# Kernel optimization log

Measured on AMD Instinct MI355X. Metric: run time of the kernel, lower is better.

## Reference

```python
import jax, jax.numpy as jnp
import numpy as np

RANK = 4
IN_FEATURES = 1024
OUT_FEATURES = 1024
ALPHA = 1.0
SCALING = ALPHA / RANK


def setup_inputs() -> dict:
    key = jax.random.key(0)
    kx, ka = jax.random.split(key)
    x = jax.random.normal(kx, (4, 8192, IN_FEATURES), dtype=jnp.float32)
    # kaiming_uniform_(a=sqrt(5)) on [rank, in_features]: bound = sqrt(3) * gain / sqrt(fan_in)
    # gain = sqrt(2/(1+a^2)) = sqrt(1/3); fan_in = in_features -> bound = 1/sqrt(in_features)
    bound = 1.0 / np.sqrt(IN_FEATURES)
    lora_A = jax.random.uniform(ka, (RANK, IN_FEATURES), dtype=jnp.float32, minval=-bound, maxval=bound)
    # original init is zeros for B; use random values so the output/gradients are non-trivial
    lora_B = jax.random.normal(jax.random.fold_in(key, 7), (OUT_FEATURES, RANK), dtype=jnp.float32) * 0.02
    return {"x": x, "lora_A": lora_A, "lora_B": lora_B}


def reference(x, lora_A, lora_B):
    # h = scaling * (x @ A^T) @ B^T   (dropout p=0 -> identity)
    h = jnp.einsum('bsi,ri->bsr', x, lora_A)      # [B, S, rank]
    h = jnp.einsum('bsr,or->bso', h, lora_B)      # [B, S, out_features]
    return h * SCALING
```

## Files before the change

### kernel.cpp

```cpp
#include <hip/hip_runtime.h>

#define IN_F 1024
#define OUT_F 1024
#define RANK 4
#define SCALING 0.25f
#define WAVES_PER_BLOCK 4
#define ROWS_PER_WAVE 8

__global__ __launch_bounds__(256, 2) void lora_fused(
    const float* __restrict__ x, const float* __restrict__ A,
    const float* __restrict__ B, float* __restrict__ out, int nrows) {
  const int lane = threadIdx.x & 63;
  const int wave = threadIdx.x >> 6;
  const int wave_id = blockIdx.x * WAVES_PER_BLOCK + wave;
  const int row0 = wave_id * ROWS_PER_WAVE;
  if (row0 >= nrows) return;

  const float4* __restrict__ A4 = (const float4*)A;
  float4 af[RANK][4];
#pragma unroll
  for (int r = 0; r < RANK; ++r)
#pragma unroll
    for (int w = 0; w < 4; ++w)
      af[r][w] = A4[r * 256 + w * 64 + lane];

  const float4* __restrict__ B4 = (const float4*)B;
  float4 bf[4][4];
#pragma unroll
  for (int w = 0; w < 4; ++w)
#pragma unroll
    for (int j = 0; j < 4; ++j)
      bf[w][j] = B4[4 * (w * 64 + lane) + j];

  float4 xv[4];
  {
    const float4* __restrict__ x4 = (const float4*)(x + (size_t)row0 * IN_F);
#pragma unroll
    for (int w = 0; w < 4; ++w) xv[w] = x4[w * 64 + lane];
  }

#pragma unroll 1
  for (int i = 0; i < ROWS_PER_WAVE; ++i) {
    const int row = row0 + i;
    if (row >= nrows) break;

    float4 xn[4];
    const bool have_next = (i + 1 < ROWS_PER_WAVE) && (row + 1 < nrows);
    if (have_next) {
      const float4* __restrict__ x4n =
          (const float4*)(x + (size_t)(row + 1) * IN_F);
#pragma unroll
      for (int w = 0; w < 4; ++w) xn[w] = x4n[w * 64 + lane];
    }

    float h[RANK];
#pragma unroll
    for (int r = 0; r < RANK; ++r) h[r] = 0.0f;
#pragma unroll
    for (int r = 0; r < RANK; ++r)
#pragma unroll
      for (int w = 0; w < 4; ++w)
        h[r] += xv[w].x * af[r][w].x + xv[w].y * af[r][w].y +
                xv[w].z * af[r][w].z + xv[w].w * af[r][w].w;

#pragma unroll
    for (int off = 32; off > 0; off >>= 1)
#pragma unroll
      for (int r = 0; r < RANK; ++r) h[r] += __shfl_xor(h[r], off, 64);

#pragma unroll
    for (int r = 0; r < RANK; ++r) h[r] *= SCALING;

    float4* __restrict__ out4 = (float4*)(out + (size_t)row * OUT_F);
#pragma unroll
    for (int w = 0; w < 4; ++w) {
      float4 res;
      res.x = h[0] * bf[w][0].x + h[1] * bf[w][0].y + h[2] * bf[w][0].z +
              h[3] * bf[w][0].w;
      res.y = h[0] * bf[w][1].x + h[1] * bf[w][1].y + h[2] * bf[w][1].z +
              h[3] * bf[w][1].w;
      res.z = h[0] * bf[w][2].x + h[1] * bf[w][2].y + h[2] * bf[w][2].z +
              h[3] * bf[w][2].w;
      res.w = h[0] * bf[w][3].x + h[1] * bf[w][3].y + h[2] * bf[w][3].z +
              h[3] * bf[w][3].w;
      out4[w * 64 + lane] = res;
    }

    if (have_next) {
#pragma unroll
      for (int w = 0; w < 4; ++w) xv[w] = xn[w];
    }
  }
}

extern "C" void kernel_launch(void* const* d_in, const int* in_sizes, int n_in,
                              void* d_out, int out_size, void* d_ws,
                              size_t ws_size, hipStream_t stream) {
  const float* x = (const float*)d_in[0];
  const float* A = (const float*)d_in[1];
  const float* B = (const float*)d_in[2];
  float* out = (float*)d_out;

  const int nrows = in_sizes[0] / IN_F;
  const int waves = (nrows + ROWS_PER_WAVE - 1) / ROWS_PER_WAVE;
  const int blocks = (waves + WAVES_PER_BLOCK - 1) / WAVES_PER_BLOCK;
  lora_fused<<<blocks, WAVES_PER_BLOCK * 64, 0, stream>>>(x, A, B, out, nrows);
}
```

Baseline: 235.3 us.

## Stage x tiles into LDS via async global_load_lds with double buffering

Restructures the kernel so each block handles a 16-row tile. x rows are streamed into LDS in 256-column chunks using the global_load_lds builtin, with double buffering and explicit waitcnt. A is kept in LDS, and the rank-4 projection is reduced over 16-lane groups. The up-projection then writes the full tile using B held in registers. The intent is to raise memory-level parallelism on the x read and to spread output writes across the whole block. The risks are hand-coded waitcnt encodings, ROW_PITCH padding alignment for the 16-byte LDS loads, and no tail handling when nrows is not a multiple of 16.

```diff
diff --git a/kernel.cpp b/kernel.cpp
--- a/kernel.cpp
+++ b/kernel.cpp
@@ -1,95 +1,116 @@
 #include <hip/hip_runtime.h>
+#include <stdint.h>
 
 #define IN_F 1024
 #define OUT_F 1024
-#define RANK 4
 #define SCALING 0.25f
-#define WAVES_PER_BLOCK 4
-#define ROWS_PER_WAVE 8
+#define TILE_ROWS 16
+#define CHUNK_COLS 256
+#define NCHUNK (IN_F / CHUNK_COLS)
+#define ROW_PITCH 260
+#define BLOCK 256
 
-__global__ __launch_bounds__(256, 2) void lora_fused(
+typedef __attribute__((address_space(3))) unsigned int as3_u32;
+typedef const __attribute__((address_space(1))) unsigned int as1_u32;
+
+__device__ __forceinline__ void row_to_lds(const float* g, const float* lds_row,
+                                           int lane) {
+  __builtin_amdgcn_global_load_lds(
+      (as1_u32*)(uintptr_t)(g + lane * 4),
+      (as3_u32*)(uint32_t)(uintptr_t)(lds_row),
+      16, 0, 0);
+}
+
+__global__ __launch_bounds__(BLOCK) void lora_tile(
     const float* __restrict__ x, const float* __restrict__ A,
     const float* __restrict__ B, float* __restrict__ out, int nrows) {
-  const int lane = threadIdx.x & 63;
-  const int wave = threadIdx.x >> 6;
-  const int wave_id = blockIdx.x * WAVES_PER_BLOCK + wave;
-  const int row0 = wave_id * ROWS_PER_WAVE;
+  __shared__ float4 As4[4 * 256];
+  __shared__ float xs[2][TILE_ROWS * ROW_PITCH];
+  __shared__ float4 hf[TILE_ROWS];
+
+  const int t = threadIdx.x;
+  const int lane = t & 63;
+  const int wave = t >> 6;
+  const int row0 = blockIdx.x * TILE_ROWS;
   if (row0 >= nrows) return;
 
+  const float4* __restrict__ B4 = (const float4*)B;
+  const float4 bf0 = B4[4 * t + 0];
+  const float4 bf1 = B4[4 * t + 1];
+  const float4 bf2 = B4[4 * t + 2];
+  const float4 bf3 = B4[4 * t + 3];
+
   const float4* __restrict__ A4 = (const float4*)A;
-  float4 af[RANK][4];
 #pragma unroll
-  for (int r = 0; r < RANK; ++r)
+  for (int k = 0; k < 4; ++k) As4[t + 256 * k] = A4[t + 256 * k];
+  __syncthreads();
+
 #pragma unroll
-    for (int w = 0; w < 4; ++w)
-      af[r][w] = A4[r * 256 + w * 64 + lane];
-
-  const float4* __restrict__ B4 = (const float4*)B;
-  float4 bf[4][4];
-#pragma unroll
-  for (int w = 0; w < 4; ++w)
-#pragma unroll
-    for (int j = 0; j < 4; ++j)
-      bf[w][j] = B4[4 * (w * 64 + lane) + j];
-
-  float4 xv[4];
-  {
-    const float4* __restrict__ x4 = (const float4*)(x + (size_t)row0 * IN_F);
-#pragma unroll
-    for (int w = 0; w < 4; ++w) xv[w] = x4[w * 64 + lane];
+  for (int r = 0; r < 4; ++r) {
+    const int row = wave * 4 + r;
+    row_to_lds(x + (size_t)(row0 + row) * IN_F, &xs[0][row * ROW_PITCH], lane);
   }
 
-#pragma unroll 1
-  for (int i = 0; i < ROWS_PER_WAVE; ++i) {
-    const int row = row0 + i;
-    if (row >= nrows) break;
+  const int lrow = lane >> 4;
+  const int seg = lane & 15;
+  const int myrow = wave * 4 + lrow;
 
-    float4 xn[4];
-    const bool have_next = (i + 1 < ROWS_PER_WAVE) && (row + 1 < nrows);
-    if (have_next) {
-      const float4* __restrict__ x4n =
-          (const float4*)(x + (size_t)(row + 1) * IN_F);
-#pragma unroll
-      for (int w = 0; w < 4; ++w) xn[w] = x4n[w * 64 + lane];
-    }
-
-    float h[RANK];
-#pragma unroll
-    for (int r = 0; r < RANK; ++r) h[r] = 0.0f;
-#pragma unroll
-    for (int r = 0; r < RANK; ++r)
-#pragma unroll
-      for (int w = 0; w < 4; ++w)
-        h[r] += xv[w].x * af[r][w].x + xv[w].y * af[r][w].y +
-                xv[w].z * af[r][w].z + xv[w].w * af[r][w].w;
+  float h0 = 0.f, h1 = 0.f, h2 = 0.f, h3 = 0.f;
 
 #pragma unroll
-    for (int off = 32; off > 0; off >>= 1)
+  for (int c = 0; c < NCHUNK; ++c) {
+    if (c + 1 < NCHUNK) {
 #pragma unroll
-      for (int r = 0; r < RANK; ++r) h[r] += __shfl_xor(h[r], off, 64);
+      for (int r = 0; r < 4; ++r) {
+        const int row = wave * 4 + r;
+        row_to_lds(x + (size_t)(row0 + row) * IN_F + (c + 1) * CHUNK_COLS,
+                   &xs[(c + 1) & 1][row * ROW_PITCH], lane);
+      }
+      __builtin_amdgcn_s_waitcnt(0xF74);
+    } else {
+      __builtin_amdgcn_s_waitcnt(0xF70);
+    }
+    __asm__ __volatile__("" ::: "memory");
+
+    const float4* __restrict__ xr4 =
+        (const float4*)&xs[c & 1][myrow * ROW_PITCH + seg * 16];
+#pragma unroll
+    for (int j = 0; j < 4; ++j) {
+      const float4 xv = xr4[j];
+      const int ai = c * 64 + seg * 4 + j;
+      const float4 a0 = As4[0 * 256 + ai];
+      const float4 a1 = As4[1 * 256 + ai];
+      const float4 a2 = As4[2 * 256 + ai];
+      const float4 a3 = As4[3 * 256 + ai];
+      h0 += xv.x * a0.x + xv.y * a0.y + xv.z * a0.z + xv.w * a0.w;
+      h1 += xv.x * a1.x + xv.y * a1.y + xv.z * a1.z + xv.w * a1.w;
+      h2 += xv.x * a2.x + xv.y * a2.y + xv.z * a2.z + xv.w * a2.w;
+      h3 += xv.x * a3.x + xv.y * a3.y + xv.z * a3.z + xv.w * a3.w;
+    }
+  }
 
 #pragma unroll
-    for (int r = 0; r < RANK; ++r) h[r] *= SCALING;
+  for (int off = 1; off < 16; off <<= 1) {
+    h0 += __shfl_xor(h0, off, 64);
+    h1 += __shfl_xor(h1, off, 64);
+    h2 += __shfl_xor(h2, off, 64);
+    h3 += __shfl_xor(h3, off, 64);
+  }
+  if (seg == 0)
+    hf[myrow] = make_float4(h0 * SCALING, h1 * SCALING, h2 * SCALING,
+                            h3 * SCALING);
+  __syncthreads();
 
-    float4* __restrict__ out4 = (float4*)(out + (size_t)row * OUT_F);
+  float4* __restrict__ out4 = (float4*)out;
 #pragma unroll
-    for (int w = 0; w < 4; ++w) {
-      float4 res;
-      res.x = h[0] * bf[w][0].x + h[1] * bf[w][0].y + h[2] * bf[w][0].z +
-              h[3] * bf[w][0].w;
-      res.y = h[0] * bf[w][1].x + h[1] * bf[w][1].y + h[2] * bf[w][1].z +
-              h[3] * bf[w][1].w;
-      res.z = h[0] * bf[w][2].x + h[1] * bf[w][2].y + h[2] * bf[w][2].z +
-              h[3] * bf[w][2].w;
-      res.w = h[0] * bf[w][3].x + h[1] * bf[w][3].y + h[2] * bf[w][3].z +
-              h[3] * bf[w][3].w;
-      out4[w * 64 + lane] = res;
-    }
-
-    if (have_next) {
-#pragma unroll
-      for (int w = 0; w < 4; ++w) xv[w] = xn[w];
-    }
+  for (int r = 0; r < TILE_ROWS; ++r) {
+    const float4 h = hf[r];
+    float4 res;
+    res.x = h.x * bf0.x + h.y * bf0.y + h.z * bf0.z + h.w * bf0.w;
+    res.y = h.x * bf1.x + h.y * bf1.y + h.z * bf1.z + h.w * bf1.w;
+    res.z = h.x * bf2.x + h.y * bf2.y + h.z * bf2.z + h.w * bf2.w;
+    res.w = h.x * bf3.x + h.y * bf3.y + h.z * bf3.z + h.w * bf3.w;
+    out4[(size_t)(row0 + r) * (OUT_F / 4) + t] = res;
   }
 }
 
@@ -102,7 +123,6 @@
   float* out = (float*)d_out;
 
   const int nrows = in_sizes[0] / IN_F;
-  const int waves = (nrows + ROWS_PER_WAVE - 1) / ROWS_PER_WAVE;
-  const int blocks = (waves + WAVES_PER_BLOCK - 1) / WAVES_PER_BLOCK;
-  lora_fused<<<blocks, WAVES_PER_BLOCK * 64, 0, stream>>>(x, A, B, out, nrows);
+  const int blocks = (nrows + TILE_ROWS - 1) / TILE_ROWS;
+  lora_tile<<<blocks, BLOCK, 0, stream>>>(x, A, B, out, nrows);
 }
```

After: 234.9 us. No clear change (-0.1%).

## Stream x in double-buffered row pairs, reload weights from cache, nontemporal stores

Applied to the files above, without the earlier changes.

Restructures the per-wave loop into a fully unrolled double-buffered schedule that loads two rows of x at a time while computing the previous pair. A and B are no longer held in registers but reloaded from cache per row, with asm barriers to keep the pointers in scalar registers. Output uses nontemporal stores, and the occupancy hint in launch bounds is dropped. The goal is more loads in flight per wave for this bandwidth-bound kernel, paid for with extra cache traffic for the weights and higher register use for the buffers.

```diff
diff --git a/kernel.cpp b/kernel.cpp
--- a/kernel.cpp
+++ b/kernel.cpp
@@ -1,94 +1,105 @@
 #include <hip/hip_runtime.h>
 
+typedef float vf4 __attribute__((ext_vector_type(4)));
+
 #define IN_F 1024
-#define OUT_F 1024
-#define RANK 4
+#define IN_F4 256
+#define OUT_F4 256
 #define SCALING 0.25f
-#define WAVES_PER_BLOCK 4
 #define ROWS_PER_WAVE 8
+#define BLOCK 256
 
-__global__ __launch_bounds__(256, 2) void lora_fused(
-    const float* __restrict__ x, const float* __restrict__ A,
-    const float* __restrict__ B, float* __restrict__ out, int nrows) {
+__device__ __forceinline__ void load_pair(const vf4* __restrict__ x4, int row,
+                                          int lane, vf4* xb) {
+#pragma unroll
+  for (int w = 0; w < 4; ++w)
+    xb[w] = x4[(size_t)row * IN_F4 + w * 64 + lane];
+#pragma unroll
+  for (int w = 0; w < 4; ++w)
+    xb[4 + w] = x4[(size_t)(row + 1) * IN_F4 + w * 64 + lane];
+}
+
+__device__ __forceinline__ void row_dot_expand(const vf4* A4, const vf4* B4,
+                                               vf4* __restrict__ out4,
+                                               const vf4* xb, int row,
+                                               int lane) {
+  __asm__("" : "+s"(A4));
+  __asm__("" : "+s"(B4));
+  float h0 = 0.f, h1 = 0.f, h2 = 0.f, h3 = 0.f;
+#pragma unroll
+  for (int w = 0; w < 4; ++w) {
+    const vf4 xv = xb[w];
+    const vf4 a0 = A4[0 * IN_F4 + w * 64 + lane];
+    const vf4 a1 = A4[1 * IN_F4 + w * 64 + lane];
+    const vf4 a2 = A4[2 * IN_F4 + w * 64 + lane];
+    const vf4 a3 = A4[3 * IN_F4 + w * 64 + lane];
+    h0 += xv.x * a0.x + xv.y * a0.y + xv.z * a0.z + xv.w * a0.w;
+    h1 += xv.x * a1.x + xv.y * a1.y + xv.z * a1.z + xv.w * a1.w;
+    h2 += xv.x * a2.x + xv.y * a2.y + xv.z * a2.z + xv.w * a2.w;
+    h3 += xv.x * a3.x + xv.y * a3.y + xv.z * a3.z + xv.w * a3.w;
+  }
+#pragma unroll
+  for (int off = 32; off > 0; off >>= 1) {
+    h0 += __shfl_xor(h0, off, 64);
+    h1 += __shfl_xor(h1, off, 64);
+    h2 += __shfl_xor(h2, off, 64);
+    h3 += __shfl_xor(h3, off, 64);
+  }
+  h0 *= SCALING; h1 *= SCALING; h2 *= SCALING; h3 *= SCALING;
+#pragma unroll
+  for (int w = 0; w < 4; ++w) {
+    const int e = 4 * (w * 64 + lane);
+    const vf4 b0 = B4[e + 0];
+    const vf4 b1 = B4[e + 1];
+    const vf4 b2 = B4[e + 2];
+    const vf4 b3 = B4[e + 3];
+    vf4 res;
+    res.x = h0 * b0.x + h1 * b0.y + h2 * b0.z + h3 * b0.w;
+    res.y = h0 * b1.x + h1 * b1.y + h2 * b1.z + h3 * b1.w;
+    res.z = h0 * b2.x + h1 * b2.y + h2 * b2.z + h3 * b2.w;
+    res.w = h0 * b3.x + h1 * b3.y + h2 * b3.z + h3 * b3.w;
+    __builtin_nontemporal_store(res, &out4[(size_t)row * OUT_F4 + w * 64 + lane]);
+  }
+}
+
+__device__ __forceinline__ void process_pair(const vf4* A4, const vf4* B4,
+                                             vf4* __restrict__ out4,
+                                             const vf4* xb, int row, int lane) {
+  row_dot_expand(A4, B4, out4, xb, row, lane);
+  row_dot_expand(A4, B4, out4, xb + 4, row + 1, lane);
+}
+
+__global__ __launch_bounds__(BLOCK) void lora_stream(
+    const float* __restrict__ xf, const float* __restrict__ Af,
+    const float* __restrict__ Bf, float* __restrict__ outf, int nrows) {
   const int lane = threadIdx.x & 63;
   const int wave = threadIdx.x >> 6;
-  const int wave_id = blockIdx.x * WAVES_PER_BLOCK + wave;
-  const int row0 = wave_id * ROWS_PER_WAVE;
+  const int wid = blockIdx.x * (BLOCK / 64) + wave;
+  const int row0 = wid * ROWS_PER_WAVE;
   if (row0 >= nrows) return;
 
-  const float4* __restrict__ A4 = (const float4*)A;
-  float4 af[RANK][4];
-#pragma unroll
-  for (int r = 0; r < RANK; ++r)
-#pragma unroll
-    for (int w = 0; w < 4; ++w)
-      af[r][w] = A4[r * 256 + w * 64 + lane];
+  const vf4* x4 = (const vf4*)xf;
+  const vf4* A4 = (const vf4*)Af;
+  const vf4* B4 = (const vf4*)Bf;
+  vf4* out4 = (vf4*)outf;
 
-  const float4* __restrict__ B4 = (const float4*)B;
-  float4 bf[4][4];
-#pragma unroll
-  for (int w = 0; w < 4; ++w)
-#pragma unroll
-    for (int j = 0; j < 4; ++j)
-      bf[w][j] = B4[4 * (w * 64 + lane) + j];
-
-  float4 xv[4];
-  {
-    const float4* __restrict__ x4 = (const float4*)(x + (size_t)row0 * IN_F);
-#pragma unroll
-    for (int w = 0; w < 4; ++w) xv[w] = x4[w * 64 + lane];
-  }
-
-#pragma unroll 1
-  for (int i = 0; i < ROWS_PER_WAVE; ++i) {
-    const int row = row0 + i;
-    if (row >= nrows) break;
-
-    float4 xn[4];
-    const bool have_next = (i + 1 < ROWS_PER_WAVE) && (row + 1 < nrows);
-    if (have_next) {
-      const float4* __restrict__ x4n =
-          (const float4*)(x + (size_t)(row + 1) * IN_F);
-#pragma unroll
-      for (int w = 0; w < 4; ++w) xn[w] = x4n[w * 64 + lane];
-    }
-
-    float h[RANK];
-#pragma unroll
-    for (int r = 0; r < RANK; ++r) h[r] = 0.0f;
-#pragma unroll
-    for (int r = 0; r < RANK; ++r)
+  if (row0 + ROWS_PER_WAVE <= nrows) {
+    vf4 bufA[8], bufB[8];
+    load_pair(x4, row0 + 0, lane, bufA);
+    load_pair(x4, row0 + 2, lane, bufB);
+    process_pair(A4, B4, out4, bufA, row0 + 0, lane);
+    load_pair(x4, row0 + 4, lane, bufA);
+    process_pair(A4, B4, out4, bufB, row0 + 2, lane);
+    load_pair(x4, row0 + 6, lane, bufB);
+    process_pair(A4, B4, out4, bufA, row0 + 4, lane);
+    process_pair(A4, B4, out4, bufB, row0 + 6, lane);
+  } else {
+    for (int row = row0; row < nrows; ++row) {
+      vf4 xb[4];
 #pragma unroll
       for (int w = 0; w < 4; ++w)
-        h[r] += xv[w].x * af[r][w].x + xv[w].y * af[r][w].y +
-                xv[w].z * af[r][w].z + xv[w].w * af[r][w].w;
-
-#pragma unroll
-    for (int off = 32; off > 0; off >>= 1)
-#pragma unroll
-      for (int r = 0; r < RANK; ++r) h[r] += __shfl_xor(h[r], off, 64);
-
-#pragma unroll
-    for (int r = 0; r < RANK; ++r) h[r] *= SCALING;
-
-    float4* __restrict__ out4 = (float4*)(out + (size_t)row * OUT_F);
-#pragma unroll
-    for (int w = 0; w < 4; ++w) {
-      float4 res;
-      res.x = h[0] * bf[w][0].x + h[1] * bf[w][0].y + h[2] * bf[w][0].z +
-              h[3] * bf[w][0].w;
-      res.y = h[0] * bf[w][1].x + h[1] * bf[w][1].y + h[2] * bf[w][1].z +
-              h[3] * bf[w][1].w;
-      res.z = h[0] * bf[w][2].x + h[1] * bf[w][2].y + h[2] * bf[w][2].z +
-              h[3] * bf[w][2].w;
-      res.w = h[0] * bf[w][3].x + h[1] * bf[w][3].y + h[2] * bf[w][3].z +
-              h[3] * bf[w][3].w;
-      out4[w * 64 + lane] = res;
-    }
-
-    if (have_next) {
-#pragma unroll
-      for (int w = 0; w < 4; ++w) xv[w] = xn[w];
+        xb[w] = x4[(size_t)row * IN_F4 + w * 64 + lane];
+      row_dot_expand(A4, B4, out4, xb, row, lane);
     }
   }
 }
@@ -103,6 +114,6 @@
 
   const int nrows = in_sizes[0] / IN_F;
   const int waves = (nrows + ROWS_PER_WAVE - 1) / ROWS_PER_WAVE;
-  const int blocks = (waves + WAVES_PER_BLOCK - 1) / WAVES_PER_BLOCK;
-  lora_fused<<<blocks, WAVES_PER_BLOCK * 64, 0, stream>>>(x, A, B, out, nrows);
+  const int blocks = (waves + (BLOCK / 64) - 1) / (BLOCK / 64);
+  lora_stream<<<blocks, BLOCK, 0, stream>>>(x, A, B, out, nrows);
 }
```

Result: no change. 237.0 us (+0.7%).
